# Performance work log

Hardware: AMD Instinct MI355X
Metric: run time of the kernel (lower is better)

The kernel has to match this reference:

```python
import jax, jax.numpy as jnp
import numpy as np


def setup_inputs() -> dict:
    key = jax.random.key(0)
    k1, k2, k3 = jax.random.split(key, 3)
    B, NLAT, NLON = 8, 721, 1440
    N = 12 * 512 * 512  # HEALPix nside=512 destination points
    x = jax.random.normal(k1, (B, NLAT, NLON), dtype=jnp.float32)
    # source lat-lon axes: 0.25-degree global grid; interpn requires ascending axes
    lon_src = jnp.arange(NLON, dtype=jnp.float32) * (360.0 / NLON)   # [0, 360)
    lat_src = jnp.linspace(-90.0, 90.0, NLAT, dtype=jnp.float32)
    # unstructured destination points: (lon, lat) pairs within the grid domain
    lon_q = jax.random.uniform(k2, (N,), dtype=jnp.float32, minval=0.0, maxval=360.0)
    lat_q = jax.random.uniform(k3, (N,), dtype=jnp.float32, minval=-90.0, maxval=90.0)
    xi = jnp.stack([lon_q, lat_q], axis=1)
    return {"x": x, "lon_src": lon_src, "lat_src": lat_src, "xi": xi}


def reference(x, lon_src, lat_src, xi):
    """Bilinear interpolation from a periodic lat-lon grid onto unstructured points.

    Faithful to scipy.interpolate.interpn([long, latg], z.T, xi, method='linear')
    after wrapping the longitude axis (append first column and lon=360).
    x: [B, nlat, nlon]; returns [N, B] (matching interpn on z.T).
    """
    nlat = lat_src.shape[0]
    nlon = lon_src.shape[0]
    # periodic wrap in longitude
    xw = jnp.concatenate([x, x[..., :1]], axis=-1)                 # [B, nlat, nlon+1]
    long = jnp.concatenate([lon_src, jnp.full((1,), 360.0, lon_src.dtype)])

    lon_q = xi[:, 0]
    lat_q = xi[:, 1]
    # cell indices (clip so i+1 / j+1 stay in range, matching interpn edge handling)
    i = jnp.clip(jnp.searchsorted(long, lon_q, side="right") - 1, 0, nlon - 1)    # [N]
    j = jnp.clip(jnp.searchsorted(lat_src, lat_q, side="right") - 1, 0, nlat - 2)  # [N]
    wlon = (lon_q - long[i]) / (long[i + 1] - long[i])             # [N]
    wlat = (lat_q - lat_src[j]) / (lat_src[j + 1] - lat_src[j])    # [N]

    # gather 4 corners: [B, N]
    v00 = xw[:, j, i]
    v10 = xw[:, j, i + 1]
    v01 = xw[:, j + 1, i]
    v11 = xw[:, j + 1, i + 1]

    out = (1.0 - wlat) * ((1.0 - wlon) * v00 + wlon * v10) \
        + wlat * ((1.0 - wlon) * v01 + wlon * v11)                 # [B, N]
    return out.T                                                   # [N, B] like interpn(z.T)
```

## Files before the change

kernel.cpp:

```cpp
#include <hip/hip_runtime.h>
#include <hip/hip_bf16.h>

#define NLAT 721
#define NLON 1440
#define NB 8
#define NROWS (NLAT - 1)
#define NCELLS (NROWS * NLON)

typedef float f32x2 __attribute__((ext_vector_type(2)));
typedef float f32x4 __attribute__((ext_vector_type(4)));

__device__ __forceinline__ unsigned pack2_bf16(float a, float b) {
    unsigned ua = __float_as_uint(a);
    unsigned ub = __float_as_uint(b);
    ua = (ua + 0x7FFFu + ((ua >> 16) & 1u)) >> 16;
    ub = (ub + 0x7FFFu + ((ub >> 16) & 1u)) >> 16;
    return ua | (ub << 16);
}
__device__ __forceinline__ float bf_lo(unsigned u) { return __uint_as_float(u << 16); }
__device__ __forceinline__ float bf_hi(unsigned u) { return __uint_as_float(u & 0xFFFF0000u); }

__device__ __forceinline__ uint4 pack8(const float* v) {
    return make_uint4(pack2_bf16(v[0], v[1]), pack2_bf16(v[2], v[3]),
                      pack2_bf16(v[4], v[5]), pack2_bf16(v[6], v[7]));
}

__device__ __forceinline__ void mul8(float* r, float w, uint4 U) {
    r[0] = w * bf_lo(U.x);  r[1] = w * bf_hi(U.x);
    r[2] = w * bf_lo(U.y);  r[3] = w * bf_hi(U.y);
    r[4] = w * bf_lo(U.z);  r[5] = w * bf_hi(U.z);
    r[6] = w * bf_lo(U.w);  r[7] = w * bf_hi(U.w);
}

__device__ __forceinline__ void accum8(float* r, float w, uint4 U) {
    r[0] = fmaf(w, bf_lo(U.x), r[0]);  r[1] = fmaf(w, bf_hi(U.x), r[1]);
    r[2] = fmaf(w, bf_lo(U.y), r[2]);  r[3] = fmaf(w, bf_hi(U.y), r[3]);
    r[4] = fmaf(w, bf_lo(U.z), r[4]);  r[5] = fmaf(w, bf_hi(U.z), r[5]);
    r[6] = fmaf(w, bf_lo(U.w), r[6]);  r[7] = fmaf(w, bf_hi(U.w), r[7]);
}

__device__ __forceinline__ void store_out_nt(float* out, size_t n, const float* r) {
    f32x4 o0 = {r[0], r[1], r[2], r[3]};
    f32x4 o1 = {r[4], r[5], r[6], r[7]};
    f32x4* o = (f32x4*)(out + n * NB);
    __builtin_nontemporal_store(o0, o);
    __builtin_nontemporal_store(o1, o + 1);
}

__device__ __forceinline__ void lat_cell(const float* s_lat, float lat,
                                         int& j, float& wlat) {
    j = (int)floorf((lat + 90.0f) * 4.0f);
    j = min(max(j, 0), NLAT - 2);
    while (j > 0 && lat < s_lat[j]) --j;
    while (j < NLAT - 2 && lat >= s_lat[j + 1]) ++j;
    float l0 = s_lat[j], l1 = s_lat[j + 1];
    wlat = (lat - l0) / (l1 - l0);
}

__device__ __forceinline__ void lon_cell(float lon, int& i, float& wlon) {
    float lon4 = lon * 4.0f;
    i = (int)floorf(lon4);
    i = min(max(i, 0), NLON - 1);
    wlon = lon4 - (float)i;
}

__global__ __launch_bounds__(256) void build_cells_kernel(
    const float* __restrict__ x,
    uint4* __restrict__ xc)
{
    int k = blockIdx.x * blockDim.x + threadIdx.x;
    if (k >= NCELLS * 4) return;
    int cell = k >> 2;
    int part = k & 3;
    int j = cell / NLON;
    int i = cell - j * NLON;

    int row = j + (part >> 1);
    int col = (part & 1) ? ((i == NLON - 1) ? 0 : i + 1) : i;

    float v[NB];
#pragma unroll
    for (int b = 0; b < NB; ++b)
        v[b] = x[((size_t)b * NLAT + row) * NLON + col];

    xc[k] = pack8(v);
}

__global__ __launch_bounds__(256) void regrid_cells_kernel(
    const uint4* __restrict__ xc,
    const float* __restrict__ lat_src,
    const float* __restrict__ xi,
    float* __restrict__ out,
    int N)
{
    __shared__ float s_lat[NLAT];
    for (int t = threadIdx.x; t < NLAT; t += blockDim.x) s_lat[t] = lat_src[t];
    __syncthreads();

    int base = blockIdx.x * (blockDim.x * 2);
    int n0 = base + threadIdx.x;
    int n1 = n0 + blockDim.x;
    if (n0 >= N) return;
    bool has2 = (n1 < N);

    f32x2 q0 = __builtin_nontemporal_load(((const f32x2*)xi) + n0);
    f32x2 q1 = has2 ? __builtin_nontemporal_load(((const f32x2*)xi) + n1)
                    : q0;

    int i0, i1p, j0, j1;
    float wlon0, wlon1, wlat0, wlat1;
    lon_cell(q0.x, i0, wlon0);
    lon_cell(q1.x, i1p, wlon1);
    lat_cell(s_lat, q0.y, j0, wlat0);
    lat_cell(s_lat, q1.y, j1, wlat1);

    const uint4* cp0 = xc + (size_t)(j0 * NLON + i0) * 4;
    const uint4* cp1 = xc + (size_t)(j1 * NLON + i1p) * 4;
    uint4 A0 = cp0[0], B0 = cp0[1], C0 = cp0[2], D0 = cp0[3];
    uint4 A1 = cp1[0], B1 = cp1[1], C1 = cp1[2], D1 = cp1[3];

    float alat0 = 1.0f - wlat0, alon0 = 1.0f - wlon0;
    float alat1 = 1.0f - wlat1, alon1 = 1.0f - wlon1;

    float r0[NB], r1[NB];
    mul8  (r0, alat0 * alon0, A0);
    accum8(r0, alat0 * wlon0, B0);
    accum8(r0, wlat0 * alon0, C0);
    accum8(r0, wlat0 * wlon0, D0);
    store_out_nt(out, (size_t)n0, r0);

    if (has2) {
        mul8  (r1, alat1 * alon1, A1);
        accum8(r1, alat1 * wlon1, B1);
        accum8(r1, wlat1 * alon1, C1);
        accum8(r1, wlat1 * wlon1, D1);
        store_out_nt(out, (size_t)n1, r1);
    }
}

__global__ __launch_bounds__(256) void build_pairs_kernel(
    const float* __restrict__ x,
    uint4* __restrict__ xp)
{
    int k = blockIdx.x * blockDim.x + threadIdx.x;
    if (k >= NCELLS * 2) return;
    int cell = k >> 1;
    int part = k & 1;
    int j = cell / NLON;
    int i = cell - j * NLON;
    int row = j + part;

    float v[NB];
#pragma unroll
    for (int b = 0; b < NB; ++b)
        v[b] = x[((size_t)b * NLAT + row) * NLON + i];

    xp[k] = pack8(v);
}

__global__ __launch_bounds__(256) void regrid_pairs_kernel(
    const uint4* __restrict__ xp,
    const float* __restrict__ lat_src,
    const float* __restrict__ xi,
    float* __restrict__ out,
    int N)
{
    __shared__ float s_lat[NLAT];
    for (int t = threadIdx.x; t < NLAT; t += blockDim.x) s_lat[t] = lat_src[t];
    __syncthreads();

    int n = blockIdx.x * blockDim.x + threadIdx.x;
    if (n >= N) return;

    f32x2 q = __builtin_nontemporal_load(((const f32x2*)xi) + n);

    int i, j;
    float wlon, wlat;
    lon_cell(q.x, i, wlon);
    lat_cell(s_lat, q.y, j, wlat);
    int i1 = (i == NLON - 1) ? 0 : i + 1;
    float alat = 1.0f - wlat, alon = 1.0f - wlon;

    const uint4* p0 = xp + (size_t)(j * NLON + i) * 2;
    const uint4* p1 = xp + (size_t)(j * NLON + i1) * 2;
    uint4 A = p0[0], C = p0[1];
    uint4 B = p1[0], D = p1[1];

    float r[NB];
    mul8  (r, alat * alon, A);
    accum8(r, alat * wlon, B);
    accum8(r, wlat * alon, C);
    accum8(r, wlat * wlon, D);

    store_out_nt(out, (size_t)n, r);
}

__global__ __launch_bounds__(256) void regrid_direct_kernel(
    const float* __restrict__ x,
    const float* __restrict__ lat_src,
    const float* __restrict__ xi,
    float* __restrict__ out,
    int N)
{
    __shared__ float s_lat[NLAT];
    for (int t = threadIdx.x; t < NLAT; t += blockDim.x) s_lat[t] = lat_src[t];
    __syncthreads();

    int n = blockIdx.x * blockDim.x + threadIdx.x;
    if (n >= N) return;

    f32x2 q = __builtin_nontemporal_load(((const f32x2*)xi) + n);

    int i, j;
    float wlon, wlat;
    lon_cell(q.x, i, wlon);
    lat_cell(s_lat, q.y, j, wlat);
    int i1 = (i == NLON - 1) ? 0 : i + 1;
    float alat = 1.0f - wlat, alon = 1.0f - wlon;

    float res[NB];
#pragma unroll
    for (int b = 0; b < NB; ++b) {
        const float* row0 = x + ((size_t)b * NLAT + j) * NLON;
        const float* row1 = row0 + NLON;
        res[b] = alat * (alon * row0[i] + wlon * row0[i1])
               + wlat * (alon * row1[i] + wlon * row1[i1]);
    }
    store_out_nt(out, (size_t)n, res);
}

extern "C" void kernel_launch(void* const* d_in, const int* in_sizes, int n_in,
                              void* d_out, int out_size, void* d_ws, size_t ws_size,
                              hipStream_t stream) {
    const float* x       = (const float*)d_in[0];
    const float* lat_src = (const float*)d_in[2];
    const float* xi      = (const float*)d_in[3];
    float* out           = (float*)d_out;

    int N = in_sizes[3] / 2;
    const size_t cell_bytes = (size_t)NCELLS * 64;
    const size_t pair_bytes = (size_t)NCELLS * 32;

    int ggrid  = (N + 255) / 256;
    int ggrid2 = (N + 511) / 512;

    if (ws_size >= cell_bytes) {
        uint4* xc = (uint4*)d_ws;
        int bgrid4 = (NCELLS * 4 + 255) / 256;
        build_cells_kernel<<<bgrid4, 256, 0, stream>>>(x, xc);
        regrid_cells_kernel<<<ggrid2, 256, 0, stream>>>(xc, lat_src, xi, out, N);
    } else if (ws_size >= pair_bytes) {
        uint4* xp = (uint4*)d_ws;
        int bgrid2 = (NCELLS * 2 + 255) / 256;
        build_pairs_kernel<<<bgrid2, 256, 0, stream>>>(x, xp);
        regrid_pairs_kernel<<<ggrid, 256, 0, stream>>>(xp, lat_src, xi, out, N);
    } else {
        regrid_direct_kernel<<<ggrid, 256, 0, stream>>>(x, lat_src, xi, out, N);
    }
}
```

Before: 228.9 us.

## Switch default path from 4-corner cell table to lat-pair table

Removes the 4-corner packed cell layout and makes the smaller lat-pair packed layout the default, halving the bytes the preprocessing kernel writes. The pairs gather kernel now handles two points per thread like the former cells kernel. In exchange each point needs two separate 32-byte gathers instead of one contiguous 64-byte read.

```diff
diff --git a/kernel.cpp b/kernel.cpp
--- a/kernel.cpp
+++ b/kernel.cpp
@@ -62,80 +62,6 @@
     i = (int)floorf(lon4);
     i = min(max(i, 0), NLON - 1);
     wlon = lon4 - (float)i;
-}
-
-__global__ __launch_bounds__(256) void build_cells_kernel(
-    const float* __restrict__ x,
-    uint4* __restrict__ xc)
-{
-    int k = blockIdx.x * blockDim.x + threadIdx.x;
-    if (k >= NCELLS * 4) return;
-    int cell = k >> 2;
-    int part = k & 3;
-    int j = cell / NLON;
-    int i = cell - j * NLON;
-
-    int row = j + (part >> 1);
-    int col = (part & 1) ? ((i == NLON - 1) ? 0 : i + 1) : i;
-
-    float v[NB];
-#pragma unroll
-    for (int b = 0; b < NB; ++b)
-        v[b] = x[((size_t)b * NLAT + row) * NLON + col];
-
-    xc[k] = pack8(v);
-}
-
-__global__ __launch_bounds__(256) void regrid_cells_kernel(
-    const uint4* __restrict__ xc,
-    const float* __restrict__ lat_src,
-    const float* __restrict__ xi,
-    float* __restrict__ out,
-    int N)
-{
-    __shared__ float s_lat[NLAT];
-    for (int t = threadIdx.x; t < NLAT; t += blockDim.x) s_lat[t] = lat_src[t];
-    __syncthreads();
-
-    int base = blockIdx.x * (blockDim.x * 2);
-    int n0 = base + threadIdx.x;
-    int n1 = n0 + blockDim.x;
-    if (n0 >= N) return;
-    bool has2 = (n1 < N);
-
-    f32x2 q0 = __builtin_nontemporal_load(((const f32x2*)xi) + n0);
-    f32x2 q1 = has2 ? __builtin_nontemporal_load(((const f32x2*)xi) + n1)
-                    : q0;
-
-    int i0, i1p, j0, j1;
-    float wlon0, wlon1, wlat0, wlat1;
-    lon_cell(q0.x, i0, wlon0);
-    lon_cell(q1.x, i1p, wlon1);
-    lat_cell(s_lat, q0.y, j0, wlat0);
-    lat_cell(s_lat, q1.y, j1, wlat1);
-
-    const uint4* cp0 = xc + (size_t)(j0 * NLON + i0) * 4;
-    const uint4* cp1 = xc + (size_t)(j1 * NLON + i1p) * 4;
-    uint4 A0 = cp0[0], B0 = cp0[1], C0 = cp0[2], D0 = cp0[3];
-    uint4 A1 = cp1[0], B1 = cp1[1], C1 = cp1[2], D1 = cp1[3];
-
-    float alat0 = 1.0f - wlat0, alon0 = 1.0f - wlon0;
-    float alat1 = 1.0f - wlat1, alon1 = 1.0f - wlon1;
-
-    float r0[NB], r1[NB];
-    mul8  (r0, alat0 * alon0, A0);
-    accum8(r0, alat0 * wlon0, B0);
-    accum8(r0, wlat0 * alon0, C0);
-    accum8(r0, wlat0 * wlon0, D0);
-    store_out_nt(out, (size_t)n0, r0);
-
-    if (has2) {
-        mul8  (r1, alat1 * alon1, A1);
-        accum8(r1, alat1 * wlon1, B1);
-        accum8(r1, wlat1 * alon1, C1);
-        accum8(r1, wlat1 * wlon1, D1);
-        store_out_nt(out, (size_t)n1, r1);
-    }
 }
 
 __global__ __launch_bounds__(256) void build_pairs_kernel(
@@ -169,30 +95,51 @@
     for (int t = threadIdx.x; t < NLAT; t += blockDim.x) s_lat[t] = lat_src[t];
     __syncthreads();
 
-    int n = blockIdx.x * blockDim.x + threadIdx.x;
-    if (n >= N) return;
-
-    f32x2 q = __builtin_nontemporal_load(((const f32x2*)xi) + n);
-
-    int i, j;
-    float wlon, wlat;
-    lon_cell(q.x, i, wlon);
-    lat_cell(s_lat, q.y, j, wlat);
-    int i1 = (i == NLON - 1) ? 0 : i + 1;
-    float alat = 1.0f - wlat, alon = 1.0f - wlon;
-
-    const uint4* p0 = xp + (size_t)(j * NLON + i) * 2;
-    const uint4* p1 = xp + (size_t)(j * NLON + i1) * 2;
-    uint4 A = p0[0], C = p0[1];
-    uint4 B = p1[0], D = p1[1];
-
-    float r[NB];
-    mul8  (r, alat * alon, A);
-    accum8(r, alat * wlon, B);
-    accum8(r, wlat * alon, C);
-    accum8(r, wlat * wlon, D);
-
-    store_out_nt(out, (size_t)n, r);
+    int base = blockIdx.x * (blockDim.x * 2);
+    int n0 = base + threadIdx.x;
+    int n1 = n0 + blockDim.x;
+    if (n0 >= N) return;
+    bool has2 = (n1 < N);
+
+    f32x2 q0 = __builtin_nontemporal_load(((const f32x2*)xi) + n0);
+    f32x2 q1 = has2 ? __builtin_nontemporal_load(((const f32x2*)xi) + n1)
+                    : q0;
+
+    int ia0, ia1, j0, j1;
+    float wlon0, wlon1, wlat0, wlat1;
+    lon_cell(q0.x, ia0, wlon0);
+    lon_cell(q1.x, ia1, wlon1);
+    lat_cell(s_lat, q0.y, j0, wlat0);
+    lat_cell(s_lat, q1.y, j1, wlat1);
+    int ib0 = (ia0 == NLON - 1) ? 0 : ia0 + 1;
+    int ib1 = (ia1 == NLON - 1) ? 0 : ia1 + 1;
+
+    const uint4* pa0 = xp + (size_t)(j0 * NLON + ia0) * 2;
+    const uint4* pb0 = xp + (size_t)(j0 * NLON + ib0) * 2;
+    const uint4* pa1 = xp + (size_t)(j1 * NLON + ia1) * 2;
+    const uint4* pb1 = xp + (size_t)(j1 * NLON + ib1) * 2;
+    uint4 A0 = pa0[0], C0 = pa0[1];
+    uint4 B0 = pb0[0], D0 = pb0[1];
+    uint4 A1 = pa1[0], C1 = pa1[1];
+    uint4 B1 = pb1[0], D1 = pb1[1];
+
+    float alat0 = 1.0f - wlat0, alon0 = 1.0f - wlon0;
+    float alat1 = 1.0f - wlat1, alon1 = 1.0f - wlon1;
+
+    float r0[NB], r1[NB];
+    mul8  (r0, alat0 * alon0, A0);
+    accum8(r0, alat0 * wlon0, B0);
+    accum8(r0, wlat0 * alon0, C0);
+    accum8(r0, wlat0 * wlon0, D0);
+    store_out_nt(out, (size_t)n0, r0);
+
+    if (has2) {
+        mul8  (r1, alat1 * alon1, A1);
+        accum8(r1, alat1 * wlon1, B1);
+        accum8(r1, wlat1 * alon1, C1);
+        accum8(r1, wlat1 * wlon1, D1);
+        store_out_nt(out, (size_t)n1, r1);
+    }
 }
 
 __global__ __launch_bounds__(256) void regrid_direct_kernel(
@@ -238,22 +185,16 @@
     float* out           = (float*)d_out;
 
     int N = in_sizes[3] / 2;
-    const size_t cell_bytes = (size_t)NCELLS * 64;
     const size_t pair_bytes = (size_t)NCELLS * 32;
 
     int ggrid  = (N + 255) / 256;
     int ggrid2 = (N + 511) / 512;
 
-    if (ws_size >= cell_bytes) {
-        uint4* xc = (uint4*)d_ws;
-        int bgrid4 = (NCELLS * 4 + 255) / 256;
-        build_cells_kernel<<<bgrid4, 256, 0, stream>>>(x, xc);
-        regrid_cells_kernel<<<ggrid2, 256, 0, stream>>>(xc, lat_src, xi, out, N);
-    } else if (ws_size >= pair_bytes) {
+    if (ws_size >= pair_bytes) {
         uint4* xp = (uint4*)d_ws;
         int bgrid2 = (NCELLS * 2 + 255) / 256;
         build_pairs_kernel<<<bgrid2, 256, 0, stream>>>(x, xp);
-        regrid_pairs_kernel<<<ggrid, 256, 0, stream>>>(xp, lat_src, xi, out, N);
+        regrid_pairs_kernel<<<ggrid2, 256, 0, stream>>>(xp, lat_src, xi, out, N);
     } else {
         regrid_direct_kernel<<<ggrid, 256, 0, stream>>>(x, lat_src, xi, out, N);
     }
```

After: 224.7 us. About the same (-1.8%).
